# Kernel optimization log

Measured on AMD Instinct MI355X. Metric: run time of the kernel, lower is better.

Reference implementation:

```python
import jax, jax.numpy as jnp
import numpy as np

P_OUT = 2048   # num_output_points
K_NN = 32      # num_neighbors
LEAK = 0.2     # LeakyReLU slope in WeightNet


def setup_inputs() -> dict:
    key = jax.random.key(0)
    k1, k2, k3, k4 = jax.random.split(key, 4)
    B, N, D, Cin, Cout, Cmid = 8, 8192, 3, 128, 256, 16
    return {
        "coordinates": jax.random.uniform(k1, (B, N, D), jnp.float32),
        "features": jax.random.normal(k2, (B, N, Cin), jnp.float32),
        "wn_w": jax.random.normal(k3, (Cmid, D), jnp.float32) * 0.1,
        "wn_b": jnp.zeros((Cmid,), jnp.float32),
        "lin_w": jax.random.normal(k4, (Cout, Cin * Cmid), jnp.float32) * 0.02,
        "lin_b": jnp.zeros((Cout,), jnp.float32),
    }


def _fps(coords, num_out):
    """Deterministic farthest point sampling (initial point = index 0)."""
    B, N, _ = coords.shape

    def step(carry, _):
        dist, far = carry
        centroid = jnp.take_along_axis(coords, far[:, None, None], axis=1)  # (B,1,D)
        d = jnp.linalg.norm(coords - centroid, axis=-1)                     # (B,N)
        dist = jnp.minimum(dist, d)
        return (dist, jnp.argmax(dist, axis=-1)), far

    init = (jnp.full((B, N), 1e10, coords.dtype), jnp.zeros((B,), jnp.int32))
    _, idx = jax.lax.scan(step, init, None, length=num_out)
    return jnp.transpose(idx)  # (B, num_out)


def _knn(k, coords, centers):
    # squared L2 via gram trick; monotone in L2 so top-k indices match torch.cdist+topk
    d2 = (jnp.sum(centers ** 2, -1)[:, :, None]
          + jnp.sum(coords ** 2, -1)[:, None, :]
          - 2.0 * jnp.einsum('bpd,bnd->bpn', centers, coords))
    _, idx = jax.lax.top_k(-d2, k)
    return idx  # (B,P,K)


_gather = jax.vmap(lambda pts, idx: pts[idx])  # index_points equivalent


def reference(coordinates, features, wn_w, wn_b, lin_w, lin_b):
    B = coordinates.shape[0]
    samp_idx = _fps(coordinates, P_OUT)                      # (B,P)
    out_coords = _gather(coordinates, samp_idx)              # (B,P,D)
    nbr_idx = _knn(K_NN, coordinates, out_coords)            # (B,P,K)
    group_coords = _gather(coordinates, nbr_idx)             # (B,P,K,D)
    centered = group_coords - out_coords[:, :, None, :]      # (B,P,K,D)
    group_feat = _gather(features, nbr_idx)                  # (B,P,K,Cin)
    # WeightNet: 1x1-conv MLP (single layer) + LeakyReLU(0.2)
    w = jax.nn.leaky_relu(jnp.einsum('bpkd,md->bpkm', centered, wn_w) + wn_b, LEAK)
    # PointConv aggregation: (B,P,Cin,K) @ (B,P,K,Cmid) -> (B,P,Cin,Cmid) -> flatten
    nf = jnp.einsum('bpkc,bpkm->bpcm', group_feat, w).reshape(B, P_OUT, -1)
    nf = nf @ lin_w.T + lin_b                                # (B,P,Cout)
    return out_coords, nf
```

## Files before the change

kernel.cpp:

```cpp
#include <hip/hip_runtime.h>
#include <hip/hip_bf16.h>

#define NB    8
#define NPTS  8192
#define P_OUT 2048
#define KNN   32
#define CIN   128
#define CMID  16
#define COUT  256

typedef __bf16 bf16x8 __attribute__((ext_vector_type(8)));
typedef float  f32x4  __attribute__((ext_vector_type(4)));
typedef float  f32x2  __attribute__((ext_vector_type(2)));

__device__ __forceinline__ float sqrt_rn_f32(float x) { return (float)sqrt((double)x); }

__device__ __forceinline__ unsigned short f2bf(float x) {
    unsigned u = __float_as_uint(x);
    return (unsigned short)((u + 0x7FFFu + ((u >> 16) & 1u)) >> 16);
}

__device__ __forceinline__ float wave_max_dpp(float x) {
    int v, t;
    v = __float_as_int(x);
    t = __builtin_amdgcn_update_dpp(v, v, 0xB1, 0xF, 0xF, false);
    x = fmaxf(x, __int_as_float(t));
    v = __float_as_int(x);
    t = __builtin_amdgcn_update_dpp(v, v, 0x4E, 0xF, 0xF, false);
    x = fmaxf(x, __int_as_float(t));
    v = __float_as_int(x);
    t = __builtin_amdgcn_update_dpp(v, v, 0x141, 0xF, 0xF, false);
    x = fmaxf(x, __int_as_float(t));
    v = __float_as_int(x);
    t = __builtin_amdgcn_update_dpp(v, v, 0x140, 0xF, 0xF, false);
    x = fmaxf(x, __int_as_float(t));
    v = __float_as_int(x);
    t = __builtin_amdgcn_update_dpp(v, v, 0x142, 0xA, 0xF, false);
    x = fmaxf(x, __int_as_float(t));
    v = __float_as_int(x);
    t = __builtin_amdgcn_update_dpp(v, v, 0x143, 0xC, 0xF, false);
    x = fmaxf(x, __int_as_float(t));
    return x;
}

__device__ __forceinline__ unsigned wave_min_dpp_u32(unsigned x) {
    unsigned t;
    t = (unsigned)__builtin_amdgcn_update_dpp((int)x, (int)x, 0xB1, 0xF, 0xF, false);
    x = (t < x) ? t : x;
    t = (unsigned)__builtin_amdgcn_update_dpp((int)x, (int)x, 0x4E, 0xF, 0xF, false);
    x = (t < x) ? t : x;
    t = (unsigned)__builtin_amdgcn_update_dpp((int)x, (int)x, 0x141, 0xF, 0xF, false);
    x = (t < x) ? t : x;
    t = (unsigned)__builtin_amdgcn_update_dpp((int)x, (int)x, 0x140, 0xF, 0xF, false);
    x = (t < x) ? t : x;
    t = (unsigned)__builtin_amdgcn_update_dpp((int)x, (int)x, 0x142, 0xA, 0xF, false);
    x = (t < x) ? t : x;
    t = (unsigned)__builtin_amdgcn_update_dpp((int)x, (int)x, 0x143, 0xC, 0xF, false);
    x = (t < x) ? t : x;
    return x;
}

__global__ __launch_bounds__(256) void prep_kernel(const float* __restrict__ coords,
                                                   const float* __restrict__ lin_w,
                                                   float2* __restrict__ zp,
                                                   unsigned short* __restrict__ lwbf) {
    const int i = blockIdx.x * 256 + threadIdx.x;
    if (i < NB * NPTS) {
        const float* pc = coords + (size_t)i * 3;
        const float x = pc[0], y = pc[1], z = pc[2];
        float t = __fmul_rn(x, x);
        t = __fadd_rn(t, __fmul_rn(y, y));
        t = __fadd_rn(t, __fmul_rn(z, z));
        zp[i] = make_float2(z, t);
    }
    if (i < COUT * CIN * CMID) lwbf[i] = f2bf(lin_w[i]);
}

__global__ __launch_bounds__(512) void fps_kernel(const float* __restrict__ coords,
                                                  float* __restrict__ out_coords) {
    #pragma clang fp contract(off)
    const int b    = blockIdx.x;
    const int tid  = threadIdx.x;
    const int lane = tid & 63;
    const float* cb = coords + (size_t)b * (NPTS * 3);
    float* outc = out_coords + (size_t)b * (P_OUT * 3);

    __shared__ unsigned long long gkey[3];

    f32x2 pxv[8], pyv[8], pzv[8], d2v[8];
    {
        float buf[48];
        const float4* g4 = (const float4*)cb;
        #pragma unroll
        for (int i = 0; i < 12; ++i) {
            float4 v = g4[tid * 12 + i];
            buf[i*4+0] = v.x; buf[i*4+1] = v.y; buf[i*4+2] = v.z; buf[i*4+3] = v.w;
        }
        #pragma unroll
        for (int i = 0; i < 8; ++i) {
            pxv[i] = f32x2{buf[(2*i)*3+0], buf[(2*i+1)*3+0]};
            pyv[i] = f32x2{buf[(2*i)*3+1], buf[(2*i+1)*3+1]};
            pzv[i] = f32x2{buf[(2*i)*3+2], buf[(2*i+1)*3+2]};
            d2v[i] = f32x2{__builtin_inff(), __builtin_inff()};
        }
    }
    if (tid == 0) { gkey[0] = 0ull; gkey[1] = 0ull; gkey[2] = 0ull; }
    float cx = cb[0], cy = cb[1], cz = cb[2];
    __syncthreads();
    const unsigned base = (unsigned)tid * 16;

    float h0x=0,h0y=0,h0z=0, h1x=0,h1y=0,h1z=0, h2x=0,h2y=0,h2z=0, h3x=0,h3y=0,h3z=0;

    for (int s = 0; s < P_OUT; ++s) {
        if ((s & 511) == tid) {
            const int k = s >> 9;
            if      (k == 0) { h0x=cx; h0y=cy; h0z=cz; }
            else if (k == 1) { h1x=cx; h1y=cy; h1z=cz; }
            else if (k == 2) { h2x=cx; h2y=cy; h2z=cz; }
            else             { h3x=cx; h3y=cy; h3z=cz; }
        }
        if (s == P_OUT - 1) break;

        const f32x2 cx2 = {cx, cx}, cy2 = {cy, cy}, cz2 = {cz, cz};
        f32x2 tmax2 = {0.0f, 0.0f};
        #pragma unroll
        for (int i = 0; i < 8; ++i) {
            const f32x2 dx = pxv[i] - cx2;
            const f32x2 dy = pyv[i] - cy2;
            const f32x2 dz = pzv[i] - cz2;
            f32x2 t = dx * dx;
            t = t + dy * dy;
            t = t + dz * dz;
            const f32x2 nd = __builtin_elementwise_min(d2v[i], t);
            d2v[i] = nd;
            tmax2 = __builtin_elementwise_max(tmax2, nd);
        }
        const float tmax = fmaxf(tmax2[0], tmax2[1]);

        const float wmaxl = wave_max_dpp(tmax);
        const float wmax  = __shfl(wmaxl, 63, 64);

        const unsigned wb = __float_as_uint(wmax);
        const float s_ = sqrt_rn_f32(wmax);
        float t_lo = wmax;
        #pragma unroll
        for (int j = 1; j <= 3; ++j) {
            const float v = __uint_as_float(wb - j);
            if (sqrt_rn_f32(v) == s_) t_lo = v;
        }

        unsigned cand = 0xFFFFFFFFu;
        #pragma unroll
        for (int i = 7; i >= 0; --i) {
            if (d2v[i][1] >= t_lo) cand = base + 2*i + 1;
            if (d2v[i][0] >= t_lo) cand = base + 2*i;
        }
        const unsigned candw = wave_min_dpp_u32(cand);
        if (lane == 63) {
            const unsigned long long key =
                ((unsigned long long)__float_as_uint(s_) << 32) | (unsigned long long)(~candw);
            atomicMax(&gkey[s % 3], key);
        }
        __syncthreads();

        if (tid == 0) gkey[(s + 2) % 3] = 0ull;

        const unsigned long long g = gkey[s % 3];
        const unsigned widx = ~((unsigned)g);
        cx = cb[widx * 3 + 0];
        cy = cb[widx * 3 + 1];
        cz = cb[widx * 3 + 2];
    }

    #pragma unroll
    for (int k = 0; k < 4; ++k) {
        const int s = tid + 512 * k;
        const float x = (k==0)?h0x:(k==1)?h1x:(k==2)?h2x:h3x;
        const float y = (k==0)?h0y:(k==1)?h1y:(k==2)?h2y:h3y;
        const float z = (k==0)?h0z:(k==1)?h1z:(k==2)?h2z:h3z;
        outc[s*3+0] = x; outc[s*3+1] = y; outc[s*3+2] = z;
    }
}

__global__ __launch_bounds__(1024) void knn_kernel(const float* __restrict__ coords,
                                                   const float2* __restrict__ zp,
                                                   const float* __restrict__ out_coords,
                                                   int* __restrict__ nbr) {
    const int b     = blockIdx.x & 7;
    const int chunk = blockIdx.x >> 3;
    const int tid   = threadIdx.x;
    const int wv    = tid >> 6, lane = tid & 63;
    __shared__ float2 sxy[NPTS];
    {
        float buf[24];
        const float4* g4 = (const float4*)(coords + (size_t)b * (NPTS * 3));
        #pragma unroll
        for (int i = 0; i < 6; ++i) {
            float4 v = g4[tid * 6 + i];
            buf[i*4+0]=v.x; buf[i*4+1]=v.y; buf[i*4+2]=v.z; buf[i*4+3]=v.w;
        }
        #pragma unroll
        for (int i = 0; i < 8; ++i)
            sxy[tid*8 + i] = make_float2(buf[i*3+0], buf[i*3+1]);
    }
    __syncthreads();
    const float2* zpb = zp + (size_t)b * NPTS;

    for (int ci = 0; ci < 4; ++ci) {
        const int p = chunk * 64 + wv * 4 + ci;
        const float* oc = out_coords + ((size_t)b * P_OUT + p) * 3;
        const float cx = oc[0], cy = oc[1], cz = oc[2];
        const float cc = __fadd_rn(__fadd_rn(__fmul_rn(cx,cx), __fmul_rn(cy,cy)), __fmul_rn(cz,cz));
        float ld2 = __builtin_inff();
        unsigned lidx = 0x7FFFFFFFu;
        for (int j0 = 0; j0 < NPTS; j0 += 64) {
            const int p2 = j0 + lane;
            const float2 xy = sxy[p2];
            const float2 zq = zpb[p2];
            const float dot = fmaf(cz, zq.x, fmaf(cy, xy.y, __fmul_rn(cx, xy.x)));
            const float d2  = __fsub_rn(__fadd_rn(cc, zq.y), __fmul_rn(2.0f, dot));
            const float    T  = __shfl(ld2, 31, 64);
            const unsigned Ti = __shfl(lidx, 31, 64);
            const bool qf = (d2 < T) || (d2 == T && (unsigned)p2 < Ti);
            unsigned long long mask = __ballot(qf);
            while (mask) {
                const int l = __ffsll(mask) - 1;
                const float    cd2  = __shfl(d2, l, 64);
                const unsigned cidx = (unsigned)(j0 + l);
                float    pv = __shfl_up(ld2, 1, 64);
                unsigned pi = __shfl_up(lidx, 1, 64);
                if (lane == 0) { pv = cd2; pi = cidx; }
                const bool mlt = (ld2 < cd2) || (ld2 == cd2 && lidx < cidx);
                const bool plt = (pv  < cd2) || (pv  == cd2 && pi   < cidx);
                ld2  = mlt ? ld2  : (plt ? cd2  : pv);
                lidx = mlt ? lidx : (plt ? cidx : pi);
                mask &= (mask - 1);
            }
        }
        if (lane < KNN) nbr[((size_t)b * P_OUT + p) * KNN + lane] = (int)lidx;
    }
}

__global__ __launch_bounds__(128) void pconv_kernel(const float* __restrict__ coords,
                                                    const float* __restrict__ feats,
                                                    const float* __restrict__ out_coords,
                                                    const int* __restrict__ nbr,
                                                    const float* __restrict__ wn_w,
                                                    const float* __restrict__ wn_b,
                                                    unsigned short* __restrict__ nf) {
    const int bp  = (blockIdx.x & 7) * P_OUT + (blockIdx.x >> 3);
    const int b   = bp >> 11;
    const int tid = threadIdx.x;
    __shared__ __align__(16) float wmat[32][16];
    __shared__ int nidx[32];
    __shared__ float ctr[3];
    if (tid < 32) nidx[tid] = nbr[(size_t)bp * KNN + tid];
    if (tid < 3)  ctr[tid]  = out_coords[(size_t)bp * 3 + tid];
    __syncthreads();
    {
        const int k  = tid >> 2;
        const int m0 = (tid & 3) * 4;
        const int n  = nidx[k];
        const float* pc = coords + ((size_t)b * NPTS + n) * 3;
        const float dx = pc[0] - ctr[0];
        const float dy = pc[1] - ctr[1];
        const float dz = pc[2] - ctr[2];
        #pragma unroll
        for (int mm = 0; mm < 4; ++mm) {
            const int m = m0 + mm;
            float a = dx * wn_w[m*3+0] + dy * wn_w[m*3+1] + dz * wn_w[m*3+2] + wn_b[m];
            wmat[k][m] = (a >= 0.0f) ? a : 0.2f * a;
        }
    }
    __syncthreads();
    const int c = tid;
    float acc[16];
    #pragma unroll
    for (int m = 0; m < 16; ++m) acc[m] = 0.0f;
    const float* fb = feats + (size_t)b * NPTS * CIN;
    #pragma unroll 4
    for (int k = 0; k < 32; ++k) {
        const float f = fb[(size_t)nidx[k] * CIN + c];
        const float4* wr = (const float4*)(&wmat[k][0]);
        const float4 w0 = wr[0], w1 = wr[1], w2 = wr[2], w3 = wr[3];
        acc[0]  += f * w0.x;  acc[1]  += f * w0.y;  acc[2]  += f * w0.z;  acc[3]  += f * w0.w;
        acc[4]  += f * w1.x;  acc[5]  += f * w1.y;  acc[6]  += f * w1.z;  acc[7]  += f * w1.w;
        acc[8]  += f * w2.x;  acc[9]  += f * w2.y;  acc[10] += f * w2.z;  acc[11] += f * w2.w;
        acc[12] += f * w3.x;  acc[13] += f * w3.y;  acc[14] += f * w3.z;  acc[15] += f * w3.w;
    }
    unsigned u[8];
    #pragma unroll
    for (int m = 0; m < 8; ++m) {
        const unsigned lo = f2bf(acc[2*m]);
        const unsigned hi = f2bf(acc[2*m+1]);
        u[m] = lo | (hi << 16);
    }
    uint4* dst = (uint4*)(nf + (size_t)bp * 2048 + c * 16);
    dst[0] = make_uint4(u[0], u[1], u[2], u[3]);
    dst[1] = make_uint4(u[4], u[5], u[6], u[7]);
}

__global__ __launch_bounds__(256) void gemm_kernel(const unsigned short* __restrict__ A,
                                                   const unsigned short* __restrict__ Bw,
                                                   const float* __restrict__ bias,
                                                   float* __restrict__ C) {
    __shared__ __align__(16) unsigned short Als[128 * 40];
    __shared__ __align__(16) unsigned short Bls[128 * 40];
    const int tid = threadIdx.x;
    const int m0  = blockIdx.x * 128;
    const int cb  = blockIdx.y;
    const int wv  = tid >> 6, lane = tid & 63;
    const int wr  = wv >> 1,  wc   = wv & 1;
    const int sr  = tid >> 1;
    const int ko  = (tid & 1) * 16;
    const int rr  = lane & 15, kg = lane >> 4;

    f32x4 acc[4][4] = {};

    for (int kt = 0; kt < 2048 / 32; ++kt) {
        const uint4* as = (const uint4*)(A  + (size_t)(m0 + sr) * 2048 + kt * 32 + ko);
        const uint4 a0 = as[0], a1 = as[1];
        const uint4* bs = (const uint4*)(Bw + (size_t)(cb * 128 + sr) * 2048 + kt * 32 + ko);
        const uint4 b0 = bs[0], b1 = bs[1];
        __syncthreads();
        *(uint4*)(&Als[sr * 40 + ko])     = a0;
        *(uint4*)(&Als[sr * 40 + ko + 8]) = a1;
        *(uint4*)(&Bls[sr * 40 + ko])     = b0;
        *(uint4*)(&Bls[sr * 40 + ko + 8]) = b1;
        __syncthreads();
        bf16x8 af[4], bfv[4];
        #pragma unroll
        for (int i = 0; i < 4; ++i)
            af[i] = *(const bf16x8*)(&Als[(wr*64 + i*16 + rr) * 40 + kg * 8]);
        #pragma unroll
        for (int j = 0; j < 4; ++j)
            bfv[j] = *(const bf16x8*)(&Bls[(wc*64 + j*16 + rr) * 40 + kg * 8]);
        #pragma unroll
        for (int i = 0; i < 4; ++i)
            #pragma unroll
            for (int j = 0; j < 4; ++j)
                acc[i][j] = __builtin_amdgcn_mfma_f32_16x16x32_bf16(af[i], bfv[j], acc[i][j], 0, 0, 0);
    }
    const int rg = lane >> 4;
    #pragma unroll
    for (int j = 0; j < 4; ++j) {
        const int col = cb * 128 + wc * 64 + j * 16 + rr;
        const float bv = bias[col];
        #pragma unroll
        for (int i = 0; i < 4; ++i) {
            const int row = m0 + wr * 64 + i * 16 + rg * 4;
            #pragma unroll
            for (int g = 0; g < 4; ++g)
                C[(size_t)(row + g) * 256 + col] = acc[i][j][g] + bv;
        }
    }
}

extern "C" void kernel_launch(void* const* d_in, const int* in_sizes, int n_in,
                              void* d_out, int out_size, void* d_ws, size_t ws_size,
                              hipStream_t stream) {
    const float* coords = (const float*)d_in[0];
    const float* feats  = (const float*)d_in[1];
    const float* wn_w   = (const float*)d_in[2];
    const float* wn_b   = (const float*)d_in[3];
    const float* lin_w  = (const float*)d_in[4];
    const float* lin_b  = (const float*)d_in[5];

    float* out        = (float*)d_out;
    float* out_coords = out;
    float* out_nf     = out + NB * P_OUT * 3;

    char* ws = (char*)d_ws;
    int*            nbr  = (int*)ws;
    float2*         zp   = (float2*)(ws + ((size_t)2  << 20));
    unsigned short* lwbf = (unsigned short*)(ws + ((size_t)2560 << 10));
    unsigned short* nf   = (unsigned short*)(ws + ((size_t)4  << 20));

    prep_kernel <<<2048, 256, 0, stream>>>(coords, lin_w, zp, lwbf);
    fps_kernel  <<<NB, 512, 0, stream>>>(coords, out_coords);
    knn_kernel  <<<256, 1024, 0, stream>>>(coords, zp, out_coords, nbr);
    pconv_kernel<<<NB * P_OUT, 128, 0, stream>>>(coords, feats, out_coords, nbr, wn_w, wn_b, nf);
    gemm_kernel <<<dim3(128, 2), 256, 0, stream>>>(nf, lwbf, lin_b, out_nf);
}
```

Before: 3.392 ms.

## Replace FPS shared atomicMax with per-wave slots and in-register argmax reduction

In the farthest-point-sampling loop, each wave now writes its best key and the winning point's coordinates into its own shared-memory slot instead of doing an atomicMax on a rotating 64-bit key. After one barrier, every thread reads all eight slots and reduces them in registers. This removes the atomic, the key reset and the dependent global reload of the centroid coordinates from the serial critical path. It also uses readlane instead of shfl and short-circuits the sqrt tie-threshold checks. The cost is more LDS reads and compares per thread on each step.

After: 3.558 ms. +4.9%, slower.

```diff
diff --git a/kernel.cpp b/kernel.cpp
--- a/kernel.cpp
+++ b/kernel.cpp
@@ -81,11 +81,11 @@
     #pragma clang fp contract(off)
     const int b    = blockIdx.x;
     const int tid  = threadIdx.x;
-    const int lane = tid & 63;
+    const int wv   = tid >> 6;
     const float* cb = coords + (size_t)b * (NPTS * 3);
     float* outc = out_coords + (size_t)b * (P_OUT * 3);
 
-    __shared__ unsigned long long gkey[3];
+    __shared__ __align__(16) unsigned wslot[8][8];
 
     f32x2 pxv[8], pyv[8], pzv[8], d2v[8];
     {
@@ -104,9 +104,7 @@
             d2v[i] = f32x2{__builtin_inff(), __builtin_inff()};
         }
     }
-    if (tid == 0) { gkey[0] = 0ull; gkey[1] = 0ull; gkey[2] = 0ull; }
     float cx = cb[0], cy = cb[1], cz = cb[2];
-    __syncthreads();
     const unsigned base = (unsigned)tid * 16;
 
     float h0x=0,h0y=0,h0z=0, h1x=0,h1y=0,h1z=0, h2x=0,h2y=0,h2z=0, h3x=0,h3y=0,h3z=0;
@@ -138,46 +136,72 @@
         const float tmax = fmaxf(tmax2[0], tmax2[1]);
 
         const float wmaxl = wave_max_dpp(tmax);
-        const float wmax  = __shfl(wmaxl, 63, 64);
+        const float wmax  = __int_as_float(__builtin_amdgcn_readlane(__float_as_int(wmaxl), 63));
 
         const unsigned wb = __float_as_uint(wmax);
         const float s_ = sqrt_rn_f32(wmax);
         float t_lo = wmax;
-        #pragma unroll
-        for (int j = 1; j <= 3; ++j) {
-            const float v = __uint_as_float(wb - j);
-            if (sqrt_rn_f32(v) == s_) t_lo = v;
+        {
+            const float v1 = __uint_as_float(wb - 1u);
+            if (sqrt_rn_f32(v1) == s_) {
+                t_lo = v1;
+                const float v2 = __uint_as_float(wb - 2u);
+                if (sqrt_rn_f32(v2) == s_) {
+                    t_lo = v2;
+                    const float v3 = __uint_as_float(wb - 3u);
+                    if (sqrt_rn_f32(v3) == s_) t_lo = v3;
+                }
+            }
         }
 
         unsigned cand = 0xFFFFFFFFu;
+        float cdx = 0.0f, cdy = 0.0f, cdz = 0.0f;
         #pragma unroll
         for (int i = 7; i >= 0; --i) {
-            if (d2v[i][1] >= t_lo) cand = base + 2*i + 1;
-            if (d2v[i][0] >= t_lo) cand = base + 2*i;
-        }
-        const unsigned candw = wave_min_dpp_u32(cand);
-        if (lane == 63) {
-            const unsigned long long key =
-                ((unsigned long long)__float_as_uint(s_) << 32) | (unsigned long long)(~candw);
-            atomicMax(&gkey[s % 3], key);
+            if (d2v[i][1] >= t_lo) { cand = base + 2*i + 1; cdx = pxv[i][1]; cdy = pyv[i][1]; cdz = pzv[i][1]; }
+            if (d2v[i][0] >= t_lo) { cand = base + 2*i;     cdx = pxv[i][0]; cdy = pyv[i][0]; cdz = pzv[i][0]; }
+        }
+        const unsigned candl = wave_min_dpp_u32(cand);
+        const unsigned candw = (unsigned)__builtin_amdgcn_readlane((int)candl, 63);
+        if (cand == candw) {
+            *(uint4*)(&wslot[wv][0]) = make_uint4(__float_as_uint(s_), ~candw,
+                                                  __float_as_uint(cdx), __float_as_uint(cdy));
+            wslot[wv][4] = __float_as_uint(cdz);
         }
         __syncthreads();
 
-        if (tid == 0) gkey[(s + 2) % 3] = 0ull;
-
-        const unsigned long long g = gkey[s % 3];
-        const unsigned widx = ~((unsigned)g);
-        cx = cb[widx * 3 + 0];
-        cy = cb[widx * 3 + 1];
-        cz = cb[widx * 3 + 2];
+        unsigned long long k[8];
+        float sx[8], sy[8], sz[8];
+        #pragma unroll
+        for (int w = 0; w < 8; ++w) {
+            const uint4 a = *(const uint4*)(&wslot[w][0]);
+            const unsigned zb = wslot[w][4];
+            k[w]  = ((unsigned long long)a.x << 32) | (unsigned long long)a.y;
+            sx[w] = __uint_as_float(a.z);
+            sy[w] = __uint_as_float(a.w);
+            sz[w] = __uint_as_float(zb);
+        }
+        unsigned long long k01 = k[0], k23 = k[2], k45 = k[4], k67 = k[6];
+        float x01 = sx[0], y01 = sy[0], z01 = sz[0];
+        float x23 = sx[2], y23 = sy[2], z23 = sz[2];
+        float x45 = sx[4], y45 = sy[4], z45 = sz[4];
+        float x67 = sx[6], y67 = sy[6], z67 = sz[6];
+        if (k[1] > k01) { k01 = k[1]; x01 = sx[1]; y01 = sy[1]; z01 = sz[1]; }
+        if (k[3] > k23) { k23 = k[3]; x23 = sx[3]; y23 = sy[3]; z23 = sz[3]; }
+        if (k[5] > k45) { k45 = k[5]; x45 = sx[5]; y45 = sy[5]; z45 = sz[5]; }
+        if (k[7] > k67) { k67 = k[7]; x67 = sx[7]; y67 = sy[7]; z67 = sz[7]; }
+        if (k23 > k01) { k01 = k23; x01 = x23; y01 = y23; z01 = z23; }
+        if (k67 > k45) { k45 = k67; x45 = x67; y45 = y67; z45 = z67; }
+        if (k45 > k01) { x01 = x45; y01 = y45; z01 = z45; }
+        cx = x01; cy = y01; cz = z01;
     }
 
     #pragma unroll
-    for (int k = 0; k < 4; ++k) {
-        const int s = tid + 512 * k;
-        const float x = (k==0)?h0x:(k==1)?h1x:(k==2)?h2x:h3x;
-        const float y = (k==0)?h0y:(k==1)?h1y:(k==2)?h2y:h3y;
-        const float z = (k==0)?h0z:(k==1)?h1z:(k==2)?h2z:h3z;
+    for (int kk = 0; kk < 4; ++kk) {
+        const int s = tid + 512 * kk;
+        const float x = (kk==0)?h0x:(kk==1)?h1x:(kk==2)?h2x:h3x;
+        const float y = (kk==0)?h0y:(kk==1)?h1y:(kk==2)?h2y:h3y;
+        const float z = (kk==0)?h0z:(kk==1)?h1z:(kk==2)?h2z:h3z;
         outc[s*3+0] = x; outc[s*3+1] = y; outc[s*3+2] = z;
     }
 }
```
